# Optimization experiments

Hardware: AMD Instinct MI355X
Metric: run time of the kernel (lower is better)

Reference implementation:

```python
import jax, jax.numpy as jnp
import numpy as np

B, N, D, R = 4, 50000, 64, 500
E_PER = 62500
E = B * E_PER


def _build_edges():
    rng = np.random.default_rng(0)
    idx = np.repeat(np.arange(B), E_PER)
    vi = rng.integers(0, N, E)
    vj = rng.integers(0, N, E)
    order = np.lexsort((vj, vi, idx))
    idx, vi, vj = idx[order], vi[order], vj[order]
    rel = rng.integers(0, R, E)
    key_vi = idx.astype(np.int64) * N + vi
    _, idx_vi = np.unique(key_vi, return_inverse=True)  # sorted -> nondecreasing segment ids
    key_vj = idx.astype(np.int64) * N + vj
    _, idx_vj = np.unique(key_vj, return_inverse=True)
    all_keys = np.concatenate([key_vi, key_vj])
    uniq_all, inv = np.unique(all_keys, return_inverse=True)
    e2vi, e2vj = inv[:E], inv[E:]
    sel = np.stack([idx, vi, vj, rel, idx_vi, idx_vj, e2vi, e2vj], axis=1).astype(np.int32)
    return sel, int(idx_vi.max() + 1), int(idx_vj.max() + 1), int(len(uniq_all))


def setup_inputs() -> dict:
    sel, n_vi_seg, n_vj_seg, n_visited = _build_edges()
    key = jax.random.key(0)
    ks = jax.random.split(key, 9)
    na = jax.random.uniform(ks[0], (B, N), jnp.float32) + 1e-6
    na = na / jnp.sum(na, axis=1, keepdims=True)
    return {
        'node_attention': na,
        'selected_edges': jnp.asarray(sel),
        'edges_y': jax.random.uniform(ks[1], (E,), jnp.float32, 0.1, 1.0),
        'hidden_con': jax.random.normal(ks[2], (n_visited, D), jnp.float32) * 0.1,
        'hidden_uncon': jax.random.normal(ks[3], (1, N, D), jnp.float32) * 0.1,
        'rel_emb': jax.random.normal(ks[4], (R, D), jnp.float32) * 0.1,
        'ws': jax.random.normal(ks[5], (8, D), jnp.float32) * (1.0 / np.sqrt(8.0)),
        'b': jax.random.normal(ks[6], (D,), jnp.float32) * 0.01,
        'out_w': jax.random.normal(ks[7], (D,), jnp.float32) * 0.3,
        'out_b': jax.random.normal(ks[8], (D,), jnp.float32) * 0.01,
        'n_vi_seg': n_vi_seg,
        'n_vj_seg': n_vj_seg,
    }


def reference(node_attention, selected_edges, edges_y, hidden_con, hidden_uncon,
              rel_emb, ws, b, out_w, out_b, n_vi_seg, n_vj_seg):
    idx, vi, vj = selected_edges[:, 0], selected_edges[:, 1], selected_edges[:, 2]
    rel, idx_vi, idx_vj = selected_edges[:, 3], selected_edges[:, 4], selected_edges[:, 5]
    e2vi, e2vj = selected_edges[:, 6], selected_edges[:, 7]

    # Node2Edge gathers
    hc_vi, hc_vj = hidden_con[e2vi], hidden_con[e2vj]        # [E, D]
    hu = hidden_uncon[0]                                     # hidden_uncon has batch 1
    hu_vi, hu_vj = hu[vi], hu[vj]                            # [E, D]
    re = rel_emb[rel]                                        # [E, D]

    # F layer: interact = [[0,3],[0,2,3],[0,4],[0,2,4],[1,3],[1,2,3],[1,4],[1,2,4]]
    terms = (hc_vi * hc_vj, hc_vi * re * hc_vj, hc_vi * hu_vj, hc_vi * re * hu_vj,
             hu_vi * hc_vj, hu_vi * re * hc_vj, hu_vi * hu_vj, hu_vi * re * hu_vj)
    f = b
    for k in range(8):
        f = f + ws[k] * terms[k]
    f = jax.nn.relu(f) * out_w + out_b                       # [E, D]
    logits = jnp.sum(f, axis=1)                              # [E]

    # NeighborSoftmax at='vi' (segment softmax)
    seg_max = jax.ops.segment_max(logits, idx_vi, num_segments=n_vi_seg)
    e = jnp.exp(logits - seg_max[idx_vi])
    es = jax.ops.segment_sum(e, idx_vi, num_segments=n_vi_seg)
    transition = e / es[idx_vi]

    # attention flow
    na_e = node_attention[idx, vi]
    ta = na_e * transition * edges_y

    # Aggregate at='vj', sum, then scatter into (B, n_nodes)
    aggr = jax.ops.segment_sum(ta, idx_vj, num_segments=n_vj_seg)
    seg_idx = jax.ops.segment_max(idx, idx_vj, num_segments=n_vj_seg)
    seg_vj = jax.ops.segment_max(vj, idx_vj, num_segments=n_vj_seg)
    Bn, Nn = node_attention.shape
    new_att = jnp.zeros((Bn, Nn), node_attention.dtype).at[seg_idx, seg_vj].add(aggr)
    return new_att / jnp.sum(new_att, axis=1, keepdims=True)
```

## Files before the change

kernel.cpp:

```cpp
#include <hip/hip_runtime.h>
#include <math.h>

#define D 64
#define CH 128
#define HALO 32
#define WSZ (CH + HALO)

__global__ void k_zero(float4* __restrict__ out4, float* __restrict__ row_sum,
                       int BN4, int Bn)
{
    const int i = blockIdx.x * 256 + threadIdx.x;
    if (i < BN4) out4[i] = make_float4(0.f, 0.f, 0.f, 0.f);
    if (i < Bn) row_sum[i] = 0.f;
}

__global__ __launch_bounds__(256) void k_fused(
    const int* __restrict__ sel, const float* __restrict__ hc,
    const float* __restrict__ hu, const float* __restrict__ re,
    const float* __restrict__ wsm, const float* __restrict__ bias,
    const float* __restrict__ out_w, const float* __restrict__ out_b,
    const float* __restrict__ na, const float* __restrict__ edges_y,
    float* __restrict__ out, float* __restrict__ row_sum,
    int E, int N)
{
    __shared__ int   s_sel[WSZ * 8];
    __shared__ float s_logit[WSZ];
    __shared__ int   s_ivi[WSZ];
    __shared__ float s_row[8];

    const int b0 = blockIdx.x * CH;
    const int Wc = min(WSZ, E - b0);

    {
        const int nint = Wc * 8;
        const int* selw = sel + (size_t)b0 * 8;
        for (int i = threadIdx.x; i < nint; i += 256) s_sel[i] = selw[i];
    }
    if (threadIdx.x < 8) s_row[threadIdx.x] = 0.f;

    const int lane = threadIdx.x & 63;
    const int g    = lane >> 4;
    const int d16  = lane & 15;
    const int wv   = threadIdx.x >> 6;

    const float4* wsm4 = (const float4*)wsm;
    float4 Wk[8];
    #pragma unroll
    for (int k = 0; k < 8; ++k) Wk[k] = wsm4[k * 16 + d16];
    const float4 Bv = ((const float4*)bias)[d16];
    const float4 Ow = ((const float4*)out_w)[d16];
    const float4 Ob = ((const float4*)out_b)[d16];
    const float* Wf  = (const float*)Wk;
    const float* Bvf = (const float*)&Bv;
    const float* Owf = (const float*)&Ow;
    const float* Obf = (const float*)&Ob;

    const float4* hc4 = (const float4*)hc;
    const float4* hu4 = (const float4*)hu;
    const float4* re4 = (const float4*)re;
    const int4*   s_sel4 = (const int4*)s_sel;

    __syncthreads();

    #pragma unroll 1
    for (int t = 0; t < WSZ / 32; ++t) {
        const int j0 = t * 32 + wv * 8 + g;
        const int j1 = j0 + 4;
        const bool v0 = (j0 < Wc);
        const bool v1 = (j1 < Wc);
        const int jc0 = v0 ? j0 : (Wc - 1);
        const int jc1 = v1 ? j1 : (Wc - 1);

        const int4 sA0 = s_sel4[jc0 * 2];
        const int4 sB0 = s_sel4[jc0 * 2 + 1];
        const int4 sA1 = s_sel4[jc1 * 2];
        const int4 sB1 = s_sel4[jc1 * 2 + 1];

        const float4 a0  = hc4[(size_t)sB0.z * 16 + d16];
        const float4 c0  = hc4[(size_t)sB0.w * 16 + d16];
        const float4 ui0 = hu4[(size_t)sA0.y * 16 + d16];
        const float4 uj0 = hu4[(size_t)sA0.z * 16 + d16];
        const float4 r0  = re4[(size_t)sA0.w * 16 + d16];
        const float4 a1  = hc4[(size_t)sB1.z * 16 + d16];
        const float4 c1  = hc4[(size_t)sB1.w * 16 + d16];
        const float4 ui1 = hu4[(size_t)sA1.y * 16 + d16];
        const float4 uj1 = hu4[(size_t)sA1.z * 16 + d16];
        const float4 r1  = re4[(size_t)sA1.w * 16 + d16];

        float acc0 = 0.f, acc1 = 0.f;
        {
            const float* ap = (const float*)&a0;  const float* cp = (const float*)&c0;
            const float* up = (const float*)&ui0; const float* vp = (const float*)&uj0;
            const float* rp = (const float*)&r0;
            #pragma unroll
            for (int k4 = 0; k4 < 4; ++k4) {
                const float hcvi = ap[k4], hcvj = cp[k4], huvi = up[k4], huvj = vp[k4], rr = rp[k4];
                const float hcr = hcvi * rr, hur = huvi * rr;
                float f = Bvf[k4];
                f += Wf[0*4+k4] * (hcvi * hcvj);
                f += Wf[1*4+k4] * (hcr  * hcvj);
                f += Wf[2*4+k4] * (hcvi * huvj);
                f += Wf[3*4+k4] * (hcr  * huvj);
                f += Wf[4*4+k4] * (huvi * hcvj);
                f += Wf[5*4+k4] * (hur  * hcvj);
                f += Wf[6*4+k4] * (huvi * huvj);
                f += Wf[7*4+k4] * (hur  * huvj);
                acc0 += fmaxf(f, 0.f) * Owf[k4] + Obf[k4];
            }
        }
        {
            const float* ap = (const float*)&a1;  const float* cp = (const float*)&c1;
            const float* up = (const float*)&ui1; const float* vp = (const float*)&uj1;
            const float* rp = (const float*)&r1;
            #pragma unroll
            for (int k4 = 0; k4 < 4; ++k4) {
                const float hcvi = ap[k4], hcvj = cp[k4], huvi = up[k4], huvj = vp[k4], rr = rp[k4];
                const float hcr = hcvi * rr, hur = huvi * rr;
                float f = Bvf[k4];
                f += Wf[0*4+k4] * (hcvi * hcvj);
                f += Wf[1*4+k4] * (hcr  * hcvj);
                f += Wf[2*4+k4] * (hcvi * huvj);
                f += Wf[3*4+k4] * (hcr  * huvj);
                f += Wf[4*4+k4] * (huvi * hcvj);
                f += Wf[5*4+k4] * (hur  * hcvj);
                f += Wf[6*4+k4] * (huvi * huvj);
                f += Wf[7*4+k4] * (hur  * huvj);
                acc1 += fmaxf(f, 0.f) * Owf[k4] + Obf[k4];
            }
        }

        #pragma unroll
        for (int off = 8; off > 0; off >>= 1) {
            acc0 += __shfl_xor(acc0, off, 64);
            acc1 += __shfl_xor(acc1, off, 64);
        }

        if (d16 == 0) {
            if (v0) { s_logit[j0] = acc0; s_ivi[j0] = sB0.x; }
            if (v1) { s_logit[j1] = acc1; s_ivi[j1] = sB1.x; }
        }
    }

    __syncthreads();

    const int ivi_prev = (b0 > 0) ? sel[((size_t)b0 - 1) * 8 + 4] : -1;

    for (int j = threadIdx.x; j < Wc; j += 256) {
        const int myivi = s_ivi[j];

        int s = j;
        while (s > 0 && s_ivi[s - 1] == myivi) --s;
        const bool genuine = (s > 0) || (myivi != ivi_prev);
        if (!genuine || s >= CH) continue;

        int en = j + 1;
        while (en < Wc && s_ivi[en] == myivi) ++en;

        float m = s_logit[j];
        for (int i = s; i < en; ++i) m = fmaxf(m, s_logit[i]);
        float sum = 0.f;
        for (int i = s; i < en; ++i) sum += __expf(s_logit[i] - m);

        const int idx = s_sel[j * 8 + 0];
        const int vi  = s_sel[j * 8 + 1];
        const int vj  = s_sel[j * 8 + 2];
        const float ta = na[(size_t)idx * N + vi]
                       * (__expf(s_logit[j] - m) / sum) * edges_y[b0 + j];

        atomicAdd(out + (size_t)idx * N + vj, ta);
        if (idx < 8) atomicAdd(&s_row[idx], ta);
        else         atomicAdd(row_sum + idx, ta);
    }

    __syncthreads();
    if (threadIdx.x < 8) {
        const float v = s_row[threadIdx.x];
        if (v != 0.f) atomicAdd(row_sum + threadIdx.x, v);
    }
}

__global__ void k_norm(float4* __restrict__ out, const float* __restrict__ row_sum, int N4) {
    const int col = blockIdx.x * blockDim.x + threadIdx.x;
    const int row = blockIdx.y;
    if (col < N4) {
        const float inv = 1.f / row_sum[row];
        const size_t i = (size_t)row * N4 + col;
        float4 v = out[i];
        v.x *= inv; v.y *= inv; v.z *= inv; v.w *= inv;
        out[i] = v;
    }
}

extern "C" void kernel_launch(void* const* d_in, const int* in_sizes, int n_in,
                              void* d_out, int out_size, void* d_ws, size_t ws_size,
                              hipStream_t stream)
{
    const float* na    = (const float*)d_in[0];
    const int*   sel   = (const int*)  d_in[1];
    const float* ey    = (const float*)d_in[2];
    const float* hc    = (const float*)d_in[3];
    const float* hu    = (const float*)d_in[4];
    const float* re    = (const float*)d_in[5];
    const float* wsm   = (const float*)d_in[6];
    const float* bias  = (const float*)d_in[7];
    const float* ow    = (const float*)d_in[8];
    const float* ob    = (const float*)d_in[9];

    float* out = (float*)d_out;

    const int E  = in_sizes[2];
    const int N  = in_sizes[4] / D;
    const int BN = in_sizes[0];
    const int Bn = BN / N;

    float* row_sum = (float*)d_ws;

    const int N4  = N / 4;
    const int BN4 = BN / 4;

    k_zero<<<(BN4 + 255) / 256, 256, 0, stream>>>((float4*)out, row_sum, BN4, Bn);

    const int nblk = (E + CH - 1) / CH;
    k_fused<<<nblk, 256, 0, stream>>>(sel, hc, hu, re, wsm, bias, ow, ob,
                                      na, ey, out, row_sum, E, N);

    dim3 ngrid((N4 + 255) / 256, Bn);
    k_norm<<<ngrid, 256, 0, stream>>>((float4*)out, row_sum, N4);
}
```

Baseline: 158.0 us.

## Double-buffer vj gathers, enlarge edge chunks, drop softmax-invariant out_b

The per-edge logit loop is restructured into a two-stage software pipeline. The hc/hu gathers for the vj side of the next 32-edge step are issued before the current step computes, to hide gather latency. The chunk size grows from 128 to 256 edges, which shrinks the share of redundant halo edges each block recomputes, at the cost of fewer, longer blocks. The out_b term is removed from the logits because a per-edge constant cancels in the segment softmax. This saves a load and some adds, but the logits themselves are no longer the reference values.

```diff
diff --git a/kernel.cpp b/kernel.cpp
--- a/kernel.cpp
+++ b/kernel.cpp
@@ -2,9 +2,10 @@
 #include <math.h>
 
 #define D 64
-#define CH 128
+#define CH 256
 #define HALO 32
 #define WSZ (CH + HALO)
+#define NT (WSZ / 32)
 
 __global__ void k_zero(float4* __restrict__ out4, float* __restrict__ row_sum,
                        int BN4, int Bn)
@@ -13,12 +14,89 @@
     if (i < BN4) out4[i] = make_float4(0.f, 0.f, 0.f, 0.f);
     if (i < Bn) row_sum[i] = 0.f;
 }
+
+__device__ __forceinline__ float edge_logit(
+    const float4 a, const float4 c, const float4 ui, const float4 uj,
+    const float4 r, const float* Wf, const float* Bvf, const float* Owf)
+{
+    const float* ap = (const float*)&a;  const float* cp = (const float*)&c;
+    const float* up = (const float*)&ui; const float* vp = (const float*)&uj;
+    const float* rp = (const float*)&r;
+    float acc = 0.f;
+    #pragma unroll
+    for (int k4 = 0; k4 < 4; ++k4) {
+        const float hcvi = ap[k4], hcvj = cp[k4], huvi = up[k4], huvj = vp[k4], rr = rp[k4];
+        const float hcr = hcvi * rr, hur = huvi * rr;
+        float f = Bvf[k4];
+        f += Wf[0*4+k4] * (hcvi * hcvj);
+        f += Wf[1*4+k4] * (hcr  * hcvj);
+        f += Wf[2*4+k4] * (hcvi * huvj);
+        f += Wf[3*4+k4] * (hcr  * huvj);
+        f += Wf[4*4+k4] * (huvi * hcvj);
+        f += Wf[5*4+k4] * (hur  * hcvj);
+        f += Wf[6*4+k4] * (huvi * huvj);
+        f += Wf[7*4+k4] * (hur  * huvj);
+        acc += fmaxf(f, 0.f) * Owf[k4];
+    }
+    return acc;
+}
+
+#define FAR_ISSUE(C0, C1, UJ0, UJ1, T)                                    \
+    {                                                                     \
+        const int jj0 = (T) * 32 + wv * 8 + g;                            \
+        const int jj1 = jj0 + 4;                                          \
+        const int jc0 = (jj0 < Wc) ? jj0 : (Wc - 1);                      \
+        const int jc1 = (jj1 < Wc) ? jj1 : (Wc - 1);                      \
+        const int e2vj0 = s_sel[jc0 * 8 + 7];                             \
+        const int vjg0  = s_sel[jc0 * 8 + 2];                             \
+        const int e2vj1 = s_sel[jc1 * 8 + 7];                             \
+        const int vjg1  = s_sel[jc1 * 8 + 2];                             \
+        C0  = hc4[(size_t)e2vj0 * 16 + d16];                              \
+        UJ0 = hu4[(size_t)vjg0  * 16 + d16];                              \
+        C1  = hc4[(size_t)e2vj1 * 16 + d16];                              \
+        UJ1 = hu4[(size_t)vjg1  * 16 + d16];                              \
+    }
+
+#define COMPUTE_STEP(C0, C1, UJ0, UJ1, T)                                 \
+    {                                                                     \
+        const int jj0 = (T) * 32 + wv * 8 + g;                            \
+        const int jj1 = jj0 + 4;                                          \
+        const bool v0 = (jj0 < Wc);                                       \
+        const bool v1 = (jj1 < Wc);                                       \
+        const int jc0 = v0 ? jj0 : (Wc - 1);                              \
+        const int jc1 = v1 ? jj1 : (Wc - 1);                              \
+        const int e2vi0 = s_sel[jc0 * 8 + 6];                             \
+        const int vig0  = s_sel[jc0 * 8 + 1];                             \
+        const int rel0  = s_sel[jc0 * 8 + 3];                             \
+        const int ivi0  = s_sel[jc0 * 8 + 4];                             \
+        const int e2vi1 = s_sel[jc1 * 8 + 6];                             \
+        const int vig1  = s_sel[jc1 * 8 + 1];                             \
+        const int rel1  = s_sel[jc1 * 8 + 3];                             \
+        const int ivi1  = s_sel[jc1 * 8 + 4];                             \
+        const float4 a0  = hc4[(size_t)e2vi0 * 16 + d16];                 \
+        const float4 ui0 = hu4[(size_t)vig0  * 16 + d16];                 \
+        const float4 r0  = re4[(size_t)rel0  * 16 + d16];                 \
+        const float4 a1  = hc4[(size_t)e2vi1 * 16 + d16];                 \
+        const float4 ui1 = hu4[(size_t)vig1  * 16 + d16];                 \
+        const float4 r1  = re4[(size_t)rel1  * 16 + d16];                 \
+        float acc0 = edge_logit(a0, C0, ui0, UJ0, r0, Wf, Bvf, Owf);      \
+        float acc1 = edge_logit(a1, C1, ui1, UJ1, r1, Wf, Bvf, Owf);      \
+        _Pragma("unroll")                                                 \
+        for (int off = 8; off > 0; off >>= 1) {                           \
+            acc0 += __shfl_xor(acc0, off, 64);                            \
+            acc1 += __shfl_xor(acc1, off, 64);                            \
+        }                                                                 \
+        if (d16 == 0) {                                                   \
+            if (v0) { s_logit[jj0] = acc0; s_ivi[jj0] = ivi0; }           \
+            if (v1) { s_logit[jj1] = acc1; s_ivi[jj1] = ivi1; }           \
+        }                                                                 \
+    }
 
 __global__ __launch_bounds__(256) void k_fused(
     const int* __restrict__ sel, const float* __restrict__ hc,
     const float* __restrict__ hu, const float* __restrict__ re,
     const float* __restrict__ wsm, const float* __restrict__ bias,
-    const float* __restrict__ out_w, const float* __restrict__ out_b,
+    const float* __restrict__ out_w,
     const float* __restrict__ na, const float* __restrict__ edges_y,
     float* __restrict__ out, float* __restrict__ row_sum,
     int E, int N)
@@ -49,97 +127,30 @@
     for (int k = 0; k < 8; ++k) Wk[k] = wsm4[k * 16 + d16];
     const float4 Bv = ((const float4*)bias)[d16];
     const float4 Ow = ((const float4*)out_w)[d16];
-    const float4 Ob = ((const float4*)out_b)[d16];
     const float* Wf  = (const float*)Wk;
     const float* Bvf = (const float*)&Bv;
     const float* Owf = (const float*)&Ow;
-    const float* Obf = (const float*)&Ob;
 
     const float4* hc4 = (const float4*)hc;
     const float4* hu4 = (const float4*)hu;
     const float4* re4 = (const float4*)re;
-    const int4*   s_sel4 = (const int4*)s_sel;
 
     __syncthreads();
 
+    float4 cA0, cA1, ujA0, ujA1;
+    float4 cB0, cB1, ujB0, ujB1;
+
+    FAR_ISSUE(cA0, cA1, ujA0, ujA1, 0);
+
+    int t = 0;
     #pragma unroll 1
-    for (int t = 0; t < WSZ / 32; ++t) {
-        const int j0 = t * 32 + wv * 8 + g;
-        const int j1 = j0 + 4;
-        const bool v0 = (j0 < Wc);
-        const bool v1 = (j1 < Wc);
-        const int jc0 = v0 ? j0 : (Wc - 1);
-        const int jc1 = v1 ? j1 : (Wc - 1);
-
-        const int4 sA0 = s_sel4[jc0 * 2];
-        const int4 sB0 = s_sel4[jc0 * 2 + 1];
-        const int4 sA1 = s_sel4[jc1 * 2];
-        const int4 sB1 = s_sel4[jc1 * 2 + 1];
-
-        const float4 a0  = hc4[(size_t)sB0.z * 16 + d16];
-        const float4 c0  = hc4[(size_t)sB0.w * 16 + d16];
-        const float4 ui0 = hu4[(size_t)sA0.y * 16 + d16];
-        const float4 uj0 = hu4[(size_t)sA0.z * 16 + d16];
-        const float4 r0  = re4[(size_t)sA0.w * 16 + d16];
-        const float4 a1  = hc4[(size_t)sB1.z * 16 + d16];
-        const float4 c1  = hc4[(size_t)sB1.w * 16 + d16];
-        const float4 ui1 = hu4[(size_t)sA1.y * 16 + d16];
-        const float4 uj1 = hu4[(size_t)sA1.z * 16 + d16];
-        const float4 r1  = re4[(size_t)sA1.w * 16 + d16];
-
-        float acc0 = 0.f, acc1 = 0.f;
-        {
-            const float* ap = (const float*)&a0;  const float* cp = (const float*)&c0;
-            const float* up = (const float*)&ui0; const float* vp = (const float*)&uj0;
-            const float* rp = (const float*)&r0;
-            #pragma unroll
-            for (int k4 = 0; k4 < 4; ++k4) {
-                const float hcvi = ap[k4], hcvj = cp[k4], huvi = up[k4], huvj = vp[k4], rr = rp[k4];
-                const float hcr = hcvi * rr, hur = huvi * rr;
-                float f = Bvf[k4];
-                f += Wf[0*4+k4] * (hcvi * hcvj);
-                f += Wf[1*4+k4] * (hcr  * hcvj);
-                f += Wf[2*4+k4] * (hcvi * huvj);
-                f += Wf[3*4+k4] * (hcr  * huvj);
-                f += Wf[4*4+k4] * (huvi * hcvj);
-                f += Wf[5*4+k4] * (hur  * hcvj);
-                f += Wf[6*4+k4] * (huvi * huvj);
-                f += Wf[7*4+k4] * (hur  * huvj);
-                acc0 += fmaxf(f, 0.f) * Owf[k4] + Obf[k4];
-            }
-        }
-        {
-            const float* ap = (const float*)&a1;  const float* cp = (const float*)&c1;
-            const float* up = (const float*)&ui1; const float* vp = (const float*)&uj1;
-            const float* rp = (const float*)&r1;
-            #pragma unroll
-            for (int k4 = 0; k4 < 4; ++k4) {
-                const float hcvi = ap[k4], hcvj = cp[k4], huvi = up[k4], huvj = vp[k4], rr = rp[k4];
-                const float hcr = hcvi * rr, hur = huvi * rr;
-                float f = Bvf[k4];
-                f += Wf[0*4+k4] * (hcvi * hcvj);
-                f += Wf[1*4+k4] * (hcr  * hcvj);
-                f += Wf[2*4+k4] * (hcvi * huvj);
-                f += Wf[3*4+k4] * (hcr  * huvj);
-                f += Wf[4*4+k4] * (huvi * hcvj);
-                f += Wf[5*4+k4] * (hur  * hcvj);
-                f += Wf[6*4+k4] * (huvi * huvj);
-                f += Wf[7*4+k4] * (hur  * huvj);
-                acc1 += fmaxf(f, 0.f) * Owf[k4] + Obf[k4];
-            }
-        }
-
-        #pragma unroll
-        for (int off = 8; off > 0; off >>= 1) {
-            acc0 += __shfl_xor(acc0, off, 64);
-            acc1 += __shfl_xor(acc1, off, 64);
-        }
-
-        if (d16 == 0) {
-            if (v0) { s_logit[j0] = acc0; s_ivi[j0] = sB0.x; }
-            if (v1) { s_logit[j1] = acc1; s_ivi[j1] = sB1.x; }
-        }
-    }
+    for (; t + 2 < NT; t += 2) {
+        FAR_ISSUE(cB0, cB1, ujB0, ujB1, t + 1);
+        COMPUTE_STEP(cA0, cA1, ujA0, ujA1, t);
+        FAR_ISSUE(cA0, cA1, ujA0, ujA1, t + 2);
+        COMPUTE_STEP(cB0, cB1, ujB0, ujB1, t + 1);
+    }
+    COMPUTE_STEP(cA0, cA1, ujA0, ujA1, NT - 1);
 
     __syncthreads();
 
@@ -204,7 +215,6 @@
     const float* wsm   = (const float*)d_in[6];
     const float* bias  = (const float*)d_in[7];
     const float* ow    = (const float*)d_in[8];
-    const float* ob    = (const float*)d_in[9];
 
     float* out = (float*)d_out;
 
@@ -221,7 +231,7 @@
     k_zero<<<(BN4 + 255) / 256, 256, 0, stream>>>((float4*)out, row_sum, BN4, Bn);
 
     const int nblk = (E + CH - 1) / CH;
-    k_fused<<<nblk, 256, 0, stream>>>(sel, hc, hu, re, wsm, bias, ow, ob,
+    k_fused<<<nblk, 256, 0, stream>>>(sel, hc, hu, re, wsm, bias, ow,
                                       na, ey, out, row_sum, E, N);
 
     dim3 ngrid((N4 + 255) / 256, Bn);
```

New measurement: 158.8 us. About the same (+0.5%).
